# Kernel optimization log

Hardware: AMD Instinct MI355X
Metric: run time of the kernel (lower is better)

## Reference

```python
import jax, jax.numpy as jnp
import numpy as np
from jax import lax


def _sobel3d_kernels():
    # Standard separable 3D Sobel: derivative d=[-1,0,1] along one axis,
    # smoothing s=[1,2,1] along the other two. Axes order (D, H, W).
    d = np.array([-1.0, 0.0, 1.0], dtype=np.float32)
    s = np.array([1.0, 2.0, 1.0], dtype=np.float32)
    kx = np.einsum('i,j,k->ijk', d, s, s)  # derivative along D
    ky = np.einsum('i,j,k->ijk', s, d, s)  # derivative along H
    kz = np.einsum('i,j,k->ijk', s, s, d)  # derivative along W
    # Stack as [Cout=3, Cin=1, 3, 3, 3] -> one conv computes x,y,z grads at once.
    return jnp.asarray(np.stack([kx, ky, kz])[:, None])


_DN = ('NCDHW', 'OIDHW', 'NCDHW')


def _conv3(x, k):
    # x: [N, 1, D, H, W], k: [3, 1, 3, 3, 3] -> [N, 3, D-2, H-2, W-2]
    # torch F.conv3d and lax conv are both cross-correlation; VALID padding.
    return lax.conv_general_dilated(x, k, (1, 1, 1), 'VALID', dimension_numbers=_DN)


def _g2(inp, k):
    # inp: [B, D, H, W, C] (channels last, as the torch module permutes)
    b, dd, hh, ww, c = inp.shape
    x = jnp.transpose(inp, (0, 4, 1, 2, 3)).reshape(b * c, 1, dd, hh, ww)
    g1 = _conv3(x, k)                                  # [B*C, 3, D-2, H-2, W-2]
    mag = jnp.sqrt(jnp.sum(g1 * g1, axis=1, keepdims=True))  # first-order magnitude
    g2 = _conv3(mag, k)                                # [B*C, 3, D-4, H-4, W-4]
    gx, gy, gz = g2[:, 0], g2[:, 1], g2[:, 2]
    # Faithful to source: sqrt(x^2 + y^2) + z^2 (note: z is squared, not inside sqrt)
    out = jnp.sqrt(gx * gx + gy * gy) + gz * gz        # [B*C, D-4, H-4, W-4]
    return out.reshape(b, c, *out.shape[1:])


def setup_inputs() -> dict:
    key = jax.random.key(0)
    k1, k2 = jax.random.split(key)
    pred = jax.random.normal(k1, (2, 64, 64, 64, 32), dtype=jnp.float32)
    hr = jax.random.normal(k2, (2, 64, 64, 64, 32), dtype=jnp.float32)
    return {'pred': pred, 'hr': hr}


def reference(pred, hr):
    k = _sobel3d_kernels()
    return jnp.mean(jnp.abs(_g2(pred, k) - _g2(hr, k)))
```

## Files before the change

kernel.cpp:

```cpp
#include <hip/hip_runtime.h>
#include <hip/hip_fp16.h>


constexpr int BDIM = 256;
constexpr size_t IN_B = 8388608;
constexpr int IN_D = 131072;
constexpr int IN_H = 2048;
constexpr int M = 62;
constexpr int F = 60;
constexpr int C = 32;
constexpr int MROW = M * C;
constexpr size_t MAGSZ = (size_t)M * M * MROW;
constexpr size_t PLANE = (size_t)M * MROW;

__device__ __forceinline__ float2 ld2(const float* p) {
    return *reinterpret_cast<const float2*>(p);
}
__device__ __forceinline__ float2 ldh2(const __half* p) {
    return __half22float2(*reinterpret_cast<const __half2*>(p));
}

struct P1W { float2 A[4], B[4], C[4]; };

__device__ __forceinline__ void p1_plane(const float* __restrict__ col, size_t zoff,
                                         const int jr[6], P1W& W)
{
    float2 SX[6], DX[6];
#pragma unroll
    for (int j = 0; j < 6; ++j) {
        const float* p = col + zoff + jr[j];
        float2 a = ld2(p), b = ld2(p + C), c = ld2(p + 2 * C);
        SX[j] = make_float2(a.x + 2.f * b.x + c.x, a.y + 2.f * b.y + c.y);
        DX[j] = make_float2(c.x - a.x, c.y - a.y);
    }
#pragma unroll
    for (int k = 0; k < 4; ++k) {
        W.A[k] = make_float2(SX[k].x + 2.f * SX[k+1].x + SX[k+2].x,
                             SX[k].y + 2.f * SX[k+1].y + SX[k+2].y);
        W.B[k] = make_float2(SX[k+2].x - SX[k].x, SX[k+2].y - SX[k].y);
        W.C[k] = make_float2(DX[k].x + 2.f * DX[k+1].x + DX[k+2].x,
                             DX[k].y + 2.f * DX[k+1].y + DX[k+2].y);
    }
}

__device__ __forceinline__ void p1_emit(const P1W& W0, const P1W& W1, const P1W& W2,
                                        __half* __restrict__ mag, size_t cb,
                                        int z, int y0, int kmax, bool xok)
{
    if (!xok) return;
#pragma unroll
    for (int k = 0; k < 4; ++k) {
        if (k < kmax) {
            float gxx = W2.A[k].x - W0.A[k].x;
            float gxy = W2.A[k].y - W0.A[k].y;
            float gyx = W0.B[k].x + 2.f * W1.B[k].x + W2.B[k].x;
            float gyy = W0.B[k].y + 2.f * W1.B[k].y + W2.B[k].y;
            float gzx = W0.C[k].x + 2.f * W1.C[k].x + W2.C[k].x;
            float gzy = W0.C[k].y + 2.f * W1.C[k].y + W2.C[k].y;
            float mx = sqrtf(gxx * gxx + gyx * gyx + gzx * gzx);
            float my = sqrtf(gxy * gxy + gyy * gyy + gzy * gzy);
            *reinterpret_cast<__half2*>(mag + ((size_t)z * M + (y0 + k)) * MROW + cb)
                = __floats2half2_rn(mx, my);
        }
    }
}

__global__ __launch_bounds__(BDIM) void sobel_mag_stream(
    const float* __restrict__ pred, const float* __restrict__ hr,
    __half* __restrict__ magbase, int bstart)
{
    const int xt = blockIdx.x & 3, yt = blockIdx.x >> 2;
    const int zc = blockIdx.y;
    const int gz = blockIdx.z;
    const int b  = bstart + (gz >> 1);
    const float* __restrict__ in  = (gz & 1) ? hr : pred;
    __half*      __restrict__ mag = magbase + (size_t)gz * MAGSZ;

    const int y0 = yt * 4;
    const int z0 = zc * 4;
    const int zn = min(4, M - z0);
    const int kmax = min(4, M - y0);
    const int xraw = xt * 16 + (threadIdx.x >> 4);
    const bool xok = xraw < M;
    const int x = min(xraw, M - 1);
    const int c2 = (threadIdx.x & 15) << 1;

    int jr[6];
#pragma unroll
    for (int j = 0; j < 6; ++j) jr[j] = min(y0 + j, 63) * IN_H;

    const float* col = in + (size_t)b * IN_B + (size_t)x * C + c2;
    const size_t cb = (size_t)x * C + c2;

    P1W W0, W1, W2;
    p1_plane(col, (size_t)(z0 + 0) * IN_D, jr, W0);
    p1_plane(col, (size_t)(z0 + 1) * IN_D, jr, W1);
    int z = 0;
    while (true) {
        p1_plane(col, (size_t)(z0 + z + 2) * IN_D, jr, W2);
        p1_emit(W0, W1, W2, mag, cb, z0 + z, y0, kmax, xok);
        if (++z >= zn) break;
        p1_plane(col, (size_t)(z0 + z + 2) * IN_D, jr, W0);
        p1_emit(W1, W2, W0, mag, cb, z0 + z, y0, kmax, xok);
        if (++z >= zn) break;
        p1_plane(col, (size_t)(z0 + z + 2) * IN_D, jr, W1);
        p1_emit(W2, W0, W1, mag, cb, z0 + z, y0, kmax, xok);
        if (++z >= zn) break;
    }
}

struct P2W { float2 A[2], B[2], C[2]; };

__device__ __forceinline__ void p2_plane(const __half* __restrict__ col, size_t zoff, P2W& W)
{
    float2 SX[4], DX[4];
#pragma unroll
    for (int j = 0; j < 4; ++j) {
        const __half* p = col + zoff + (size_t)j * MROW;
        float2 a = ldh2(p), b = ldh2(p + C), c = ldh2(p + 2 * C);
        SX[j] = make_float2(a.x + 2.f * b.x + c.x, a.y + 2.f * b.y + c.y);
        DX[j] = make_float2(c.x - a.x, c.y - a.y);
    }
#pragma unroll
    for (int k = 0; k < 2; ++k) {
        W.A[k] = make_float2(SX[k].x + 2.f * SX[k+1].x + SX[k+2].x,
                             SX[k].y + 2.f * SX[k+1].y + SX[k+2].y);
        W.B[k] = make_float2(SX[k+2].x - SX[k].x, SX[k+2].y - SX[k].y);
        W.C[k] = make_float2(DX[k].x + 2.f * DX[k+1].x + DX[k+2].x,
                             DX[k].y + 2.f * DX[k+1].y + DX[k+2].y);
    }
}

__device__ __forceinline__ void p2_emit(const P2W& P0, const P2W& P1, const P2W& P2,
                                        const P2W& H0, const P2W& H1, const P2W& H2,
                                        float& acc)
{
#pragma unroll
    for (int k = 0; k < 2; ++k) {
        float gxPx = P2.A[k].x - P0.A[k].x;
        float gxPy = P2.A[k].y - P0.A[k].y;
        float gyPx = P0.B[k].x + 2.f * P1.B[k].x + P2.B[k].x;
        float gyPy = P0.B[k].y + 2.f * P1.B[k].y + P2.B[k].y;
        float gzPx = P0.C[k].x + 2.f * P1.C[k].x + P2.C[k].x;
        float gzPy = P0.C[k].y + 2.f * P1.C[k].y + P2.C[k].y;
        float gxHx = H2.A[k].x - H0.A[k].x;
        float gxHy = H2.A[k].y - H0.A[k].y;
        float gyHx = H0.B[k].x + 2.f * H1.B[k].x + H2.B[k].x;
        float gyHy = H0.B[k].y + 2.f * H1.B[k].y + H2.B[k].y;
        float gzHx = H0.C[k].x + 2.f * H1.C[k].x + H2.C[k].x;
        float gzHy = H0.C[k].y + 2.f * H1.C[k].y + H2.C[k].y;
        float oPx = sqrtf(gxPx * gxPx + gyPx * gyPx) + gzPx * gzPx;
        float oPy = sqrtf(gxPy * gxPy + gyPy * gyPy) + gzPy * gzPy;
        float oHx = sqrtf(gxHx * gxHx + gyHx * gyHx) + gzHx * gzHx;
        float oHy = sqrtf(gxHy * gxHy + gyHy * gyHy) + gzHy * gzHy;
        acc += fabsf(oPx - oHx) + fabsf(oPy - oHy);
    }
}

__global__ __launch_bounds__(BDIM) void sobel2_stream(
    const __half* __restrict__ magbase, float* __restrict__ partial, int bstart)
{
    const int xt = blockIdx.x & 3, yt = blockIdx.x >> 2;
    const int zc = blockIdx.y;
    const int b  = bstart + blockIdx.z;
    const __half* __restrict__ magP = magbase + (size_t)(2 * blockIdx.z) * MAGSZ;
    const __half* __restrict__ magH = magP + MAGSZ;
    const int y0 = yt * 2;
    const int z0 = zc * 4;
    const int xraw = xt * 16 + (threadIdx.x >> 4);
    const bool xok = xraw < F;
    const int x = min(xraw, F - 1);
    const int c2 = (threadIdx.x & 15) << 1;

    const size_t colo = (size_t)y0 * MROW + (size_t)x * C + c2;
    const __half* colP = magP + colo;
    const __half* colH = magH + colo;

    P2W P0, P1, P2, H0, H1, H2;
    p2_plane(colP, (size_t)(z0 + 0) * PLANE, P0);
    p2_plane(colH, (size_t)(z0 + 0) * PLANE, H0);
    p2_plane(colP, (size_t)(z0 + 1) * PLANE, P1);
    p2_plane(colH, (size_t)(z0 + 1) * PLANE, H1);
    float acc = 0.f;
    int z = 0;
    while (true) {
        p2_plane(colP, (size_t)(z0 + z + 2) * PLANE, P2);
        p2_plane(colH, (size_t)(z0 + z + 2) * PLANE, H2);
        if (xok) p2_emit(P0, P1, P2, H0, H1, H2, acc);
        if (++z >= 4) break;
        p2_plane(colP, (size_t)(z0 + z + 2) * PLANE, P0);
        p2_plane(colH, (size_t)(z0 + z + 2) * PLANE, H0);
        if (xok) p2_emit(P1, P2, P0, H1, H2, H0, acc);
        if (++z >= 4) break;
        p2_plane(colP, (size_t)(z0 + z + 2) * PLANE, P1);
        p2_plane(colH, (size_t)(z0 + z + 2) * PLANE, H1);
        if (xok) p2_emit(P2, P0, P1, H2, H0, H1, acc);
        if (++z >= 4) break;
    }

    for (int o = 32; o > 0; o >>= 1) acc += __shfl_down(acc, o, 64);
    __shared__ float sred[BDIM / 64];
    const int lane = threadIdx.x & 63, wv = threadIdx.x >> 6;
    if (lane == 0) sred[wv] = acc;
    __syncthreads();
    if (threadIdx.x == 0) {
        float t = 0.f;
#pragma unroll
        for (int i = 0; i < BDIM / 64; ++i) t += sred[i];
        partial[(size_t)b * 1800 + (size_t)zc * 120 + blockIdx.x] = t;
    }
}

__global__ __launch_bounds__(BDIM) void finalize_kernel(
    const float* __restrict__ partial, float* __restrict__ out)
{
    double a = 0.0;
    for (int i = threadIdx.x; i < 3600; i += BDIM) a += (double)partial[i];
    for (int o = 32; o > 0; o >>= 1) a += __shfl_down(a, o, 64);
    __shared__ double sd[BDIM / 64];
    const int lane = threadIdx.x & 63, wv = threadIdx.x >> 6;
    if (lane == 0) sd[wv] = a;
    __syncthreads();
    if (threadIdx.x == 0) {
        double t = 0.0;
#pragma unroll
        for (int i = 0; i < BDIM / 64; ++i) t += sd[i];
        out[0] = (float)(t / 13824000.0);
    }
}

extern "C" void kernel_launch(void* const* d_in, const int* in_sizes, int n_in,
                              void* d_out, int out_size, void* d_ws, size_t ws_size,
                              hipStream_t stream)
{
    const float* pred = (const float*)d_in[0];
    const float* hr   = (const float*)d_in[1];

    float* partial = (float*)d_ws;
    __half* magbase = (__half*)((char*)d_ws + 65536);

    const bool merged = ws_size >= (size_t)65536 + 4 * MAGSZ * sizeof(__half);
    if (merged) {
        sobel_mag_stream<<<dim3(64, 16, 4), BDIM, 0, stream>>>(pred, hr, magbase, 0);
        sobel2_stream<<<dim3(120, 15, 2), BDIM, 0, stream>>>(magbase, partial, 0);
    } else {
        for (int b = 0; b < 2; ++b) {
            sobel_mag_stream<<<dim3(64, 16, 2), BDIM, 0, stream>>>(pred, hr, magbase, b);
            sobel2_stream<<<dim3(120, 15, 1), BDIM, 0, stream>>>(magbase, partial, b);
        }
    }
    finalize_kernel<<<1, BDIM, 0, stream>>>(partial, (float*)d_out);
}
```

Before: 247.6 us.

## Software-prefetch next z-plane loads and retile both Sobel stream kernels

Both stencil kernels now split each plane's work into an issue step (raw global loads into registers) and a reduce step. The next plane's loads are issued before the current output is computed, so memory latency overlaps with arithmetic. Tiling also changes: pass 1 goes from 4 y-rows by 4 z-planes to 2 y-rows by 8 z-planes (grid 124x8), and pass 2 from 4 to 6 z-planes (grid 120x10), with partial indexing adjusted to match. Fewer y-rows per block means more redundant halo reads in y, and the extra prefetch registers may lower occupancy.

```diff
diff --git a/kernel.cpp b/kernel.cpp
--- a/kernel.cpp
+++ b/kernel.cpp
@@ -16,52 +16,58 @@
 __device__ __forceinline__ float2 ld2(const float* p) {
     return *reinterpret_cast<const float2*>(p);
 }
-__device__ __forceinline__ float2 ldh2(const __half* p) {
-    return __half22float2(*reinterpret_cast<const __half2*>(p));
-}
-
-struct P1W { float2 A[4], B[4], C[4]; };
-
-__device__ __forceinline__ void p1_plane(const float* __restrict__ col, size_t zoff,
-                                         const int jr[6], P1W& W)
-{
-    float2 SX[6], DX[6];
-#pragma unroll
-    for (int j = 0; j < 6; ++j) {
-        const float* p = col + zoff + jr[j];
-        float2 a = ld2(p), b = ld2(p + C), c = ld2(p + 2 * C);
+
+struct Raw1 { float2 v[12]; };
+struct P1W  { float2 A[2], B[2], Cc[2]; };
+
+__device__ __forceinline__ void p1_issue(const float* __restrict__ pbase,
+                                         int zplane, int y0, int lo, Raw1& r)
+{
+#pragma unroll
+    for (int j = 0; j < 4; ++j) {
+        const float* rowp = pbase + (size_t)zplane * IN_D + (size_t)(y0 + j) * IN_H;
+        r.v[j * 3 + 0] = ld2(rowp + lo);
+        r.v[j * 3 + 1] = ld2(rowp + lo + C);
+        r.v[j * 3 + 2] = ld2(rowp + lo + 2 * C);
+    }
+}
+
+__device__ __forceinline__ void p1_reduce(const Raw1& r, P1W& W)
+{
+    float2 SX[4], DX[4];
+#pragma unroll
+    for (int j = 0; j < 4; ++j) {
+        float2 a = r.v[j * 3], b = r.v[j * 3 + 1], c = r.v[j * 3 + 2];
         SX[j] = make_float2(a.x + 2.f * b.x + c.x, a.y + 2.f * b.y + c.y);
         DX[j] = make_float2(c.x - a.x, c.y - a.y);
     }
 #pragma unroll
-    for (int k = 0; k < 4; ++k) {
-        W.A[k] = make_float2(SX[k].x + 2.f * SX[k+1].x + SX[k+2].x,
-                             SX[k].y + 2.f * SX[k+1].y + SX[k+2].y);
-        W.B[k] = make_float2(SX[k+2].x - SX[k].x, SX[k+2].y - SX[k].y);
-        W.C[k] = make_float2(DX[k].x + 2.f * DX[k+1].x + DX[k+2].x,
-                             DX[k].y + 2.f * DX[k+1].y + DX[k+2].y);
+    for (int k = 0; k < 2; ++k) {
+        W.A[k]  = make_float2(SX[k].x + 2.f * SX[k+1].x + SX[k+2].x,
+                              SX[k].y + 2.f * SX[k+1].y + SX[k+2].y);
+        W.B[k]  = make_float2(SX[k+2].x - SX[k].x, SX[k+2].y - SX[k].y);
+        W.Cc[k] = make_float2(DX[k].x + 2.f * DX[k+1].x + DX[k+2].x,
+                              DX[k].y + 2.f * DX[k+1].y + DX[k+2].y);
     }
 }
 
 __device__ __forceinline__ void p1_emit(const P1W& W0, const P1W& W1, const P1W& W2,
-                                        __half* __restrict__ mag, size_t cb,
-                                        int z, int y0, int kmax, bool xok)
+                                        __half* __restrict__ mag, int z, int y0,
+                                        int lo, bool xok)
 {
     if (!xok) return;
 #pragma unroll
-    for (int k = 0; k < 4; ++k) {
-        if (k < kmax) {
-            float gxx = W2.A[k].x - W0.A[k].x;
-            float gxy = W2.A[k].y - W0.A[k].y;
-            float gyx = W0.B[k].x + 2.f * W1.B[k].x + W2.B[k].x;
-            float gyy = W0.B[k].y + 2.f * W1.B[k].y + W2.B[k].y;
-            float gzx = W0.C[k].x + 2.f * W1.C[k].x + W2.C[k].x;
-            float gzy = W0.C[k].y + 2.f * W1.C[k].y + W2.C[k].y;
-            float mx = sqrtf(gxx * gxx + gyx * gyx + gzx * gzx);
-            float my = sqrtf(gxy * gxy + gyy * gyy + gzy * gzy);
-            *reinterpret_cast<__half2*>(mag + ((size_t)z * M + (y0 + k)) * MROW + cb)
-                = __floats2half2_rn(mx, my);
-        }
+    for (int k = 0; k < 2; ++k) {
+        float gxx = W2.A[k].x - W0.A[k].x;
+        float gxy = W2.A[k].y - W0.A[k].y;
+        float gyx = W0.B[k].x + 2.f * W1.B[k].x + W2.B[k].x;
+        float gyy = W0.B[k].y + 2.f * W1.B[k].y + W2.B[k].y;
+        float gzx = W0.Cc[k].x + 2.f * W1.Cc[k].x + W2.Cc[k].x;
+        float gzy = W0.Cc[k].y + 2.f * W1.Cc[k].y + W2.Cc[k].y;
+        float mx = sqrtf(gxx * gxx + gyx * gyx + gzx * gzx);
+        float my = sqrtf(gxy * gxy + gyy * gyy + gzy * gzy);
+        *reinterpret_cast<__half2*>(mag + ((size_t)z * M + (y0 + k)) * MROW + lo)
+            = __floats2half2_rn(mx, my);
     }
 }
 
@@ -76,58 +82,77 @@
     const float* __restrict__ in  = (gz & 1) ? hr : pred;
     __half*      __restrict__ mag = magbase + (size_t)gz * MAGSZ;
 
-    const int y0 = yt * 4;
-    const int z0 = zc * 4;
-    const int zn = min(4, M - z0);
-    const int kmax = min(4, M - y0);
+    const int y0 = yt * 2;
+    const int z0 = zc * 8;
+    const int zn = min(8, M - z0);
     const int xraw = xt * 16 + (threadIdx.x >> 4);
     const bool xok = xraw < M;
     const int x = min(xraw, M - 1);
-    const int c2 = (threadIdx.x & 15) << 1;
-
-    int jr[6];
-#pragma unroll
-    for (int j = 0; j < 6; ++j) jr[j] = min(y0 + j, 63) * IN_H;
-
-    const float* col = in + (size_t)b * IN_B + (size_t)x * C + c2;
-    const size_t cb = (size_t)x * C + c2;
-
+    const int lo = x * C + ((threadIdx.x & 15) << 1);
+
+    const float* pbase = in + (size_t)b * IN_B;
+
+    Raw1 r;
     P1W W0, W1, W2;
-    p1_plane(col, (size_t)(z0 + 0) * IN_D, jr, W0);
-    p1_plane(col, (size_t)(z0 + 1) * IN_D, jr, W1);
+    p1_issue(pbase, z0 + 0, y0, lo, r); p1_reduce(r, W0);
+    p1_issue(pbase, z0 + 1, y0, lo, r); p1_reduce(r, W1);
+    p1_issue(pbase, z0 + 2, y0, lo, r); p1_reduce(r, W2);
     int z = 0;
-    while (true) {
-        p1_plane(col, (size_t)(z0 + z + 2) * IN_D, jr, W2);
-        p1_emit(W0, W1, W2, mag, cb, z0 + z, y0, kmax, xok);
-        if (++z >= zn) break;
-        p1_plane(col, (size_t)(z0 + z + 2) * IN_D, jr, W0);
-        p1_emit(W1, W2, W0, mag, cb, z0 + z, y0, kmax, xok);
-        if (++z >= zn) break;
-        p1_plane(col, (size_t)(z0 + z + 2) * IN_D, jr, W1);
-        p1_emit(W2, W0, W1, mag, cb, z0 + z, y0, kmax, xok);
-        if (++z >= zn) break;
-    }
-}
-
-struct P2W { float2 A[2], B[2], C[2]; };
-
-__device__ __forceinline__ void p2_plane(const __half* __restrict__ col, size_t zoff, P2W& W)
+    for (;;) {
+        bool more = (z + 1 < zn);
+        if (more) p1_issue(pbase, z0 + z + 3, y0, lo, r);
+        p1_emit(W0, W1, W2, mag, z0 + z, y0, lo, xok);
+        if (!more) break;
+        ++z;
+        p1_reduce(r, W0);
+        more = (z + 1 < zn);
+        if (more) p1_issue(pbase, z0 + z + 3, y0, lo, r);
+        p1_emit(W1, W2, W0, mag, z0 + z, y0, lo, xok);
+        if (!more) break;
+        ++z;
+        p1_reduce(r, W1);
+        more = (z + 1 < zn);
+        if (more) p1_issue(pbase, z0 + z + 3, y0, lo, r);
+        p1_emit(W2, W0, W1, mag, z0 + z, y0, lo, xok);
+        if (!more) break;
+        ++z;
+        p1_reduce(r, W2);
+    }
+}
+
+struct Raw2 { __half2 v[12]; };
+struct P2W  { float2 A[2], B[2], Cc[2]; };
+
+__device__ __forceinline__ void p2_issue(const __half* __restrict__ mbase,
+                                         int zplane, int y0, int lo, Raw2& r)
+{
+#pragma unroll
+    for (int j = 0; j < 4; ++j) {
+        const __half* rowp = mbase + (size_t)zplane * PLANE + (size_t)(y0 + j) * MROW;
+        r.v[j * 3 + 0] = *reinterpret_cast<const __half2*>(rowp + lo);
+        r.v[j * 3 + 1] = *reinterpret_cast<const __half2*>(rowp + lo + C);
+        r.v[j * 3 + 2] = *reinterpret_cast<const __half2*>(rowp + lo + 2 * C);
+    }
+}
+
+__device__ __forceinline__ void p2_reduce(const Raw2& r, P2W& W)
 {
     float2 SX[4], DX[4];
 #pragma unroll
     for (int j = 0; j < 4; ++j) {
-        const __half* p = col + zoff + (size_t)j * MROW;
-        float2 a = ldh2(p), b = ldh2(p + C), c = ldh2(p + 2 * C);
+        float2 a = __half22float2(r.v[j * 3]);
+        float2 b = __half22float2(r.v[j * 3 + 1]);
+        float2 c = __half22float2(r.v[j * 3 + 2]);
         SX[j] = make_float2(a.x + 2.f * b.x + c.x, a.y + 2.f * b.y + c.y);
         DX[j] = make_float2(c.x - a.x, c.y - a.y);
     }
 #pragma unroll
     for (int k = 0; k < 2; ++k) {
-        W.A[k] = make_float2(SX[k].x + 2.f * SX[k+1].x + SX[k+2].x,
-                             SX[k].y + 2.f * SX[k+1].y + SX[k+2].y);
-        W.B[k] = make_float2(SX[k+2].x - SX[k].x, SX[k+2].y - SX[k].y);
-        W.C[k] = make_float2(DX[k].x + 2.f * DX[k+1].x + DX[k+2].x,
-                             DX[k].y + 2.f * DX[k+1].y + DX[k+2].y);
+        W.A[k]  = make_float2(SX[k].x + 2.f * SX[k+1].x + SX[k+2].x,
+                              SX[k].y + 2.f * SX[k+1].y + SX[k+2].y);
+        W.B[k]  = make_float2(SX[k+2].x - SX[k].x, SX[k+2].y - SX[k].y);
+        W.Cc[k] = make_float2(DX[k].x + 2.f * DX[k+1].x + DX[k+2].x,
+                              DX[k].y + 2.f * DX[k+1].y + DX[k+2].y);
     }
 }
 
@@ -141,14 +166,14 @@
         float gxPy = P2.A[k].y - P0.A[k].y;
         float gyPx = P0.B[k].x + 2.f * P1.B[k].x + P2.B[k].x;
         float gyPy = P0.B[k].y + 2.f * P1.B[k].y + P2.B[k].y;
-        float gzPx = P0.C[k].x + 2.f * P1.C[k].x + P2.C[k].x;
-        float gzPy = P0.C[k].y + 2.f * P1.C[k].y + P2.C[k].y;
+        float gzPx = P0.Cc[k].x + 2.f * P1.Cc[k].x + P2.Cc[k].x;
+        float gzPy = P0.Cc[k].y + 2.f * P1.Cc[k].y + P2.Cc[k].y;
         float gxHx = H2.A[k].x - H0.A[k].x;
         float gxHy = H2.A[k].y - H0.A[k].y;
         float gyHx = H0.B[k].x + 2.f * H1.B[k].x + H2.B[k].x;
         float gyHy = H0.B[k].y + 2.f * H1.B[k].y + H2.B[k].y;
-        float gzHx = H0.C[k].x + 2.f * H1.C[k].x + H2.C[k].x;
-        float gzHy = H0.C[k].y + 2.f * H1.C[k].y + H2.C[k].y;
+        float gzHx = H0.Cc[k].x + 2.f * H1.Cc[k].x + H2.Cc[k].x;
+        float gzHy = H0.Cc[k].y + 2.f * H1.Cc[k].y + H2.Cc[k].y;
         float oPx = sqrtf(gxPx * gxPx + gyPx * gyPx) + gzPx * gzPx;
         float oPy = sqrtf(gxPy * gxPy + gyPy * gyPy) + gzPy * gzPy;
         float oHx = sqrtf(gxHx * gxHx + gyHx * gyHx) + gzHx * gzHx;
@@ -165,37 +190,48 @@
     const int b  = bstart + blockIdx.z;
     const __half* __restrict__ magP = magbase + (size_t)(2 * blockIdx.z) * MAGSZ;
     const __half* __restrict__ magH = magP + MAGSZ;
+
     const int y0 = yt * 2;
-    const int z0 = zc * 4;
+    const int z0 = zc * 6;
+    const int zn = 6;
     const int xraw = xt * 16 + (threadIdx.x >> 4);
     const bool xok = xraw < F;
     const int x = min(xraw, F - 1);
-    const int c2 = (threadIdx.x & 15) << 1;
-
-    const size_t colo = (size_t)y0 * MROW + (size_t)x * C + c2;
-    const __half* colP = magP + colo;
-    const __half* colH = magH + colo;
-
+    const int lo = x * C + ((threadIdx.x & 15) << 1);
+
+    Raw2 rp, rh;
     P2W P0, P1, P2, H0, H1, H2;
-    p2_plane(colP, (size_t)(z0 + 0) * PLANE, P0);
-    p2_plane(colH, (size_t)(z0 + 0) * PLANE, H0);
-    p2_plane(colP, (size_t)(z0 + 1) * PLANE, P1);
-    p2_plane(colH, (size_t)(z0 + 1) * PLANE, H1);
+    p2_issue(magP, z0 + 0, y0, lo, rp); p2_issue(magH, z0 + 0, y0, lo, rh);
+    p2_reduce(rp, P0); p2_reduce(rh, H0);
+    p2_issue(magP, z0 + 1, y0, lo, rp); p2_issue(magH, z0 + 1, y0, lo, rh);
+    p2_reduce(rp, P1); p2_reduce(rh, H1);
+    p2_issue(magP, z0 + 2, y0, lo, rp); p2_issue(magH, z0 + 2, y0, lo, rh);
+    p2_reduce(rp, P2); p2_reduce(rh, H2);
+
     float acc = 0.f;
     int z = 0;
-    while (true) {
-        p2_plane(colP, (size_t)(z0 + z + 2) * PLANE, P2);
-        p2_plane(colH, (size_t)(z0 + z + 2) * PLANE, H2);
+    for (;;) {
+        bool more = (z + 1 < zn);
+        if (more) { p2_issue(magP, z0 + z + 3, y0, lo, rp);
+                    p2_issue(magH, z0 + z + 3, y0, lo, rh); }
         if (xok) p2_emit(P0, P1, P2, H0, H1, H2, acc);
-        if (++z >= 4) break;
-        p2_plane(colP, (size_t)(z0 + z + 2) * PLANE, P0);
-        p2_plane(colH, (size_t)(z0 + z + 2) * PLANE, H0);
+        if (!more) break;
+        ++z;
+        p2_reduce(rp, P0); p2_reduce(rh, H0);
+        more = (z + 1 < zn);
+        if (more) { p2_issue(magP, z0 + z + 3, y0, lo, rp);
+                    p2_issue(magH, z0 + z + 3, y0, lo, rh); }
         if (xok) p2_emit(P1, P2, P0, H1, H2, H0, acc);
-        if (++z >= 4) break;
-        p2_plane(colP, (size_t)(z0 + z + 2) * PLANE, P1);
-        p2_plane(colH, (size_t)(z0 + z + 2) * PLANE, H1);
+        if (!more) break;
+        ++z;
+        p2_reduce(rp, P1); p2_reduce(rh, H1);
+        more = (z + 1 < zn);
+        if (more) { p2_issue(magP, z0 + z + 3, y0, lo, rp);
+                    p2_issue(magH, z0 + z + 3, y0, lo, rh); }
         if (xok) p2_emit(P2, P0, P1, H2, H0, H1, acc);
-        if (++z >= 4) break;
+        if (!more) break;
+        ++z;
+        p2_reduce(rp, P2); p2_reduce(rh, H2);
     }
 
     for (int o = 32; o > 0; o >>= 1) acc += __shfl_down(acc, o, 64);
@@ -207,7 +243,7 @@
         float t = 0.f;
 #pragma unroll
         for (int i = 0; i < BDIM / 64; ++i) t += sred[i];
-        partial[(size_t)b * 1800 + (size_t)zc * 120 + blockIdx.x] = t;
+        partial[(size_t)b * 1200 + (size_t)zc * 120 + blockIdx.x] = t;
     }
 }
 
@@ -215,7 +251,7 @@
     const float* __restrict__ partial, float* __restrict__ out)
 {
     double a = 0.0;
-    for (int i = threadIdx.x; i < 3600; i += BDIM) a += (double)partial[i];
+    for (int i = threadIdx.x; i < 2400; i += BDIM) a += (double)partial[i];
     for (int o = 32; o > 0; o >>= 1) a += __shfl_down(a, o, 64);
     __shared__ double sd[BDIM / 64];
     const int lane = threadIdx.x & 63, wv = threadIdx.x >> 6;
@@ -241,12 +277,12 @@
 
     const bool merged = ws_size >= (size_t)65536 + 4 * MAGSZ * sizeof(__half);
     if (merged) {
-        sobel_mag_stream<<<dim3(64, 16, 4), BDIM, 0, stream>>>(pred, hr, magbase, 0);
-        sobel2_stream<<<dim3(120, 15, 2), BDIM, 0, stream>>>(magbase, partial, 0);
+        sobel_mag_stream<<<dim3(124, 8, 4), BDIM, 0, stream>>>(pred, hr, magbase, 0);
+        sobel2_stream<<<dim3(120, 10, 2), BDIM, 0, stream>>>(magbase, partial, 0);
     } else {
         for (int b = 0; b < 2; ++b) {
-            sobel_mag_stream<<<dim3(64, 16, 2), BDIM, 0, stream>>>(pred, hr, magbase, b);
-            sobel2_stream<<<dim3(120, 15, 1), BDIM, 0, stream>>>(magbase, partial, b);
+            sobel_mag_stream<<<dim3(124, 8, 2), BDIM, 0, stream>>>(pred, hr, magbase, b);
+            sobel2_stream<<<dim3(120, 10, 1), BDIM, 0, stream>>>(magbase, partial, b);
         }
     }
     finalize_kernel<<<1, BDIM, 0, stream>>>(partial, (float*)d_out);
```

Result: slower. 253.1 us (+2.2%).

## Stage input planes through LDS and lengthen z-chunks in both Sobel passes

Applied to the files above, without the earlier changes.

Both stencil kernels now cooperatively load each z-plane tile (with x/y halo) into padded shared memory using wide vector loads, then each thread reads its 3x3 neighbourhood from LDS instead of issuing redundant overlapping global loads. Z-chunk length grows from 4 to 8 in the first pass and 6 in the second, reducing halo re-reads across blocks, and the partial-sum grid shrinks to match. This cuts global-memory traffic and redundant loads, but adds two block barriers per plane and serialises load and compute with no double buffering. It also reduces the number of blocks, which lowers occupancy and parallelism.

```diff
diff --git a/kernel.cpp b/kernel.cpp
--- a/kernel.cpp
+++ b/kernel.cpp
@@ -13,62 +13,91 @@
 constexpr size_t MAGSZ = (size_t)M * M * MROW;
 constexpr size_t PLANE = (size_t)M * MROW;
 
-__device__ __forceinline__ float2 ld2(const float* p) {
-    return *reinterpret_cast<const float2*>(p);
-}
-__device__ __forceinline__ float2 ldh2(const __half* p) {
-    return __half22float2(*reinterpret_cast<const __half2*>(p));
-}
-
-struct P1W { float2 A[4], B[4], C[4]; };
-
-__device__ __forceinline__ void p1_plane(const float* __restrict__ col, size_t zoff,
-                                         const int jr[6], P1W& W)
+constexpr int GS1 = 34;
+constexpr int RS1 = 18 * GS1;
+constexpr int GS2 = 36;
+constexpr int RS2 = 18 * GS2;
+constexpr int VS2 = 4 * RS2;
+
+__device__ __forceinline__ float2 sm3(float2 a, float2 b, float2 c) {
+    return make_float2(a.x + 2.f * b.x + c.x, a.y + 2.f * b.y + c.y);
+}
+__device__ __forceinline__ float2 df2(float2 a, float2 c) {
+    return make_float2(c.x - a.x, c.y - a.y);
+}
+
+struct P1W { float2 A[4], B[4], Cc[4]; };
+
+__device__ __forceinline__ void p1_stage(const float* __restrict__ pbase, int zp,
+                                         int y0, int x0, float* __restrict__ lds,
+                                         int tid)
+{
+#pragma unroll
+    for (int k = 0; k < 4; ++k) {
+        int i = tid + k * BDIM;
+        if (i < 864) {
+            int row = i / 144;
+            int rem = i - row * 144;
+            int g   = rem >> 3;
+            int off = (rem & 7) << 2;
+            int ry  = min(y0 + row, 63);
+            int gx  = min(x0 + g, 63);
+            float4 v = *reinterpret_cast<const float4*>(
+                pbase + (size_t)zp * IN_D + (size_t)ry * IN_H + gx * C + off);
+            float* d = lds + row * RS1 + g * GS1 + off;
+            *reinterpret_cast<float2*>(d)     = make_float2(v.x, v.y);
+            *reinterpret_cast<float2*>(d + 2) = make_float2(v.z, v.w);
+        }
+    }
+}
+
+__device__ __forceinline__ void p1_reduce(const float* __restrict__ lds,
+                                          int xl, int cl, P1W& W)
 {
     float2 SX[6], DX[6];
 #pragma unroll
     for (int j = 0; j < 6; ++j) {
-        const float* p = col + zoff + jr[j];
-        float2 a = ld2(p), b = ld2(p + C), c = ld2(p + 2 * C);
-        SX[j] = make_float2(a.x + 2.f * b.x + c.x, a.y + 2.f * b.y + c.y);
-        DX[j] = make_float2(c.x - a.x, c.y - a.y);
+        const float* r = lds + j * RS1 + xl * GS1 + 2 * cl;
+        float2 a = *reinterpret_cast<const float2*>(r);
+        float2 b = *reinterpret_cast<const float2*>(r + GS1);
+        float2 c = *reinterpret_cast<const float2*>(r + 2 * GS1);
+        SX[j] = sm3(a, b, c);
+        DX[j] = df2(a, c);
     }
 #pragma unroll
     for (int k = 0; k < 4; ++k) {
-        W.A[k] = make_float2(SX[k].x + 2.f * SX[k+1].x + SX[k+2].x,
-                             SX[k].y + 2.f * SX[k+1].y + SX[k+2].y);
-        W.B[k] = make_float2(SX[k+2].x - SX[k].x, SX[k+2].y - SX[k].y);
-        W.C[k] = make_float2(DX[k].x + 2.f * DX[k+1].x + DX[k+2].x,
-                             DX[k].y + 2.f * DX[k+1].y + DX[k+2].y);
+        W.A[k]  = sm3(SX[k], SX[k + 1], SX[k + 2]);
+        W.B[k]  = df2(SX[k], SX[k + 2]);
+        W.Cc[k] = sm3(DX[k], DX[k + 1], DX[k + 2]);
     }
 }
 
 __device__ __forceinline__ void p1_emit(const P1W& W0, const P1W& W1, const P1W& W2,
-                                        __half* __restrict__ mag, size_t cb,
-                                        int z, int y0, int kmax, bool xok)
-{
-    if (!xok) return;
+                                        __half* __restrict__ mag, int z, int y0,
+                                        int xo, int cl, int kmax, bool xok)
+{
 #pragma unroll
     for (int k = 0; k < 4; ++k) {
         if (k < kmax) {
-            float gxx = W2.A[k].x - W0.A[k].x;
-            float gxy = W2.A[k].y - W0.A[k].y;
-            float gyx = W0.B[k].x + 2.f * W1.B[k].x + W2.B[k].x;
-            float gyy = W0.B[k].y + 2.f * W1.B[k].y + W2.B[k].y;
-            float gzx = W0.C[k].x + 2.f * W1.C[k].x + W2.C[k].x;
-            float gzy = W0.C[k].y + 2.f * W1.C[k].y + W2.C[k].y;
-            float mx = sqrtf(gxx * gxx + gyx * gyx + gzx * gzx);
-            float my = sqrtf(gxy * gxy + gyy * gyy + gzy * gzy);
-            *reinterpret_cast<__half2*>(mag + ((size_t)z * M + (y0 + k)) * MROW + cb)
-                = __floats2half2_rn(mx, my);
+            float2 gx = df2(W0.A[k], W2.A[k]);
+            float2 gy = sm3(W0.B[k], W1.B[k], W2.B[k]);
+            float2 gz = sm3(W0.Cc[k], W1.Cc[k], W2.Cc[k]);
+            float mx = sqrtf(gx.x * gx.x + gy.x * gy.x + gz.x * gz.x);
+            float my = sqrtf(gx.y * gx.y + gy.y * gy.y + gz.y * gz.y);
+            if (xok)
+                *reinterpret_cast<__half2*>(
+                    mag + ((size_t)z * M + (y0 + k)) * MROW + xo * C + 2 * cl)
+                    = __floats2half2_rn(mx, my);
         }
     }
 }
 
-__global__ __launch_bounds__(BDIM) void sobel_mag_stream(
+__global__ __launch_bounds__(BDIM) void sobel_mag_lds(
     const float* __restrict__ pred, const float* __restrict__ hr,
     __half* __restrict__ magbase, int bstart)
 {
+    __shared__ float lds[6 * RS1];
+
     const int xt = blockIdx.x & 3, yt = blockIdx.x >> 2;
     const int zc = blockIdx.y;
     const int gz = blockIdx.z;
@@ -76,58 +105,99 @@
     const float* __restrict__ in  = (gz & 1) ? hr : pred;
     __half*      __restrict__ mag = magbase + (size_t)gz * MAGSZ;
 
-    const int y0 = yt * 4;
-    const int z0 = zc * 4;
-    const int zn = min(4, M - z0);
+    const int x0 = xt * 16, y0 = yt * 4;
+    const int z0 = zc * 8;
+    const int zn = min(8, M - z0);
     const int kmax = min(4, M - y0);
-    const int xraw = xt * 16 + (threadIdx.x >> 4);
-    const bool xok = xraw < M;
-    const int x = min(xraw, M - 1);
-    const int c2 = (threadIdx.x & 15) << 1;
-
-    int jr[6];
-#pragma unroll
-    for (int j = 0; j < 6; ++j) jr[j] = min(y0 + j, 63) * IN_H;
-
-    const float* col = in + (size_t)b * IN_B + (size_t)x * C + c2;
-    const size_t cb = (size_t)x * C + c2;
+    const int tid = threadIdx.x;
+    const int xl = tid >> 4;
+    const int cl = tid & 15;
+    const int xo = x0 + xl;
+    const bool xok = xo < M;
+
+    const float* pbase = in + (size_t)b * IN_B;
 
     P1W W0, W1, W2;
-    p1_plane(col, (size_t)(z0 + 0) * IN_D, jr, W0);
-    p1_plane(col, (size_t)(z0 + 1) * IN_D, jr, W1);
-    int z = 0;
-    while (true) {
-        p1_plane(col, (size_t)(z0 + z + 2) * IN_D, jr, W2);
-        p1_emit(W0, W1, W2, mag, cb, z0 + z, y0, kmax, xok);
-        if (++z >= zn) break;
-        p1_plane(col, (size_t)(z0 + z + 2) * IN_D, jr, W0);
-        p1_emit(W1, W2, W0, mag, cb, z0 + z, y0, kmax, xok);
-        if (++z >= zn) break;
-        p1_plane(col, (size_t)(z0 + z + 2) * IN_D, jr, W1);
-        p1_emit(W2, W0, W1, mag, cb, z0 + z, y0, kmax, xok);
-        if (++z >= zn) break;
-    }
-}
-
-struct P2W { float2 A[2], B[2], C[2]; };
-
-__device__ __forceinline__ void p2_plane(const __half* __restrict__ col, size_t zoff, P2W& W)
+    p1_stage(pbase, z0 + 0, y0, x0, lds, tid);
+    __syncthreads();
+    p1_reduce(lds, xl, cl, W0);
+    __syncthreads();
+    p1_stage(pbase, z0 + 1, y0, x0, lds, tid);
+    __syncthreads();
+    p1_reduce(lds, xl, cl, W1);
+    __syncthreads();
+
+    int zi = 2;
+    for (;;) {
+        p1_stage(pbase, z0 + zi, y0, x0, lds, tid);
+        __syncthreads();
+        p1_reduce(lds, xl, cl, W2);
+        __syncthreads();
+        p1_emit(W0, W1, W2, mag, z0 + zi - 2, y0, xo, cl, kmax, xok);
+        if (++zi >= zn + 2) break;
+
+        p1_stage(pbase, z0 + zi, y0, x0, lds, tid);
+        __syncthreads();
+        p1_reduce(lds, xl, cl, W0);
+        __syncthreads();
+        p1_emit(W1, W2, W0, mag, z0 + zi - 2, y0, xo, cl, kmax, xok);
+        if (++zi >= zn + 2) break;
+
+        p1_stage(pbase, z0 + zi, y0, x0, lds, tid);
+        __syncthreads();
+        p1_reduce(lds, xl, cl, W1);
+        __syncthreads();
+        p1_emit(W2, W0, W1, mag, z0 + zi - 2, y0, xo, cl, kmax, xok);
+        if (++zi >= zn + 2) break;
+    }
+}
+
+struct P2W { float2 A[2], B[2], Cc[2]; };
+
+__device__ __forceinline__ void p2_stage(const __half* __restrict__ magP,
+                                         const __half* __restrict__ magH,
+                                         int zp, int y0, int x0,
+                                         __half* __restrict__ lds, int tid)
+{
+#pragma unroll
+    for (int k = 0; k < 5; ++k) {
+        int i = tid + k * BDIM;
+        if (i < 1152) {
+            int vol = (i >= 576) ? 1 : 0;
+            int rem = i - vol * 576;
+            int row = rem / 144;
+            int rem2 = rem - row * 144;
+            int g   = rem2 >> 3;
+            int off = (rem2 & 7) << 2;
+            const __half* src = (vol ? magH : magP)
+                + (size_t)zp * PLANE + (size_t)(y0 + row) * MROW
+                + min(x0 + g, M - 1) * C + off;
+            uint2 v = *reinterpret_cast<const uint2*>(src);
+            unsigned* d = reinterpret_cast<unsigned*>(
+                lds + vol * VS2 + row * RS2 + g * GS2 + off);
+            d[0] = v.x; d[1] = v.y;
+        }
+    }
+}
+
+__device__ __forceinline__ void p2_reduce(const __half* __restrict__ lds,
+                                          int xl, int cl, P2W& W)
 {
     float2 SX[4], DX[4];
 #pragma unroll
     for (int j = 0; j < 4; ++j) {
-        const __half* p = col + zoff + (size_t)j * MROW;
-        float2 a = ldh2(p), b = ldh2(p + C), c = ldh2(p + 2 * C);
-        SX[j] = make_float2(a.x + 2.f * b.x + c.x, a.y + 2.f * b.y + c.y);
-        DX[j] = make_float2(c.x - a.x, c.y - a.y);
+        const __half* r = lds + j * RS2 + xl * GS2 + 2 * cl;
+        float2 a = __half22float2(*reinterpret_cast<const __half2*>(r));
+        float2 b = __half22float2(*reinterpret_cast<const __half2*>(r + GS2));
+        float2 c = __half22float2(*reinterpret_cast<const __half2*>(r + 2 * GS2));
+        SX[j] = sm3(a, b, c);
+        DX[j] = df2(a, c);
     }
 #pragma unroll
     for (int k = 0; k < 2; ++k) {
-        W.A[k] = make_float2(SX[k].x + 2.f * SX[k+1].x + SX[k+2].x,
-                             SX[k].y + 2.f * SX[k+1].y + SX[k+2].y);
-        W.B[k] = make_float2(SX[k+2].x - SX[k].x, SX[k+2].y - SX[k].y);
-        W.C[k] = make_float2(DX[k].x + 2.f * DX[k+1].x + DX[k+2].x,
-                             DX[k].y + 2.f * DX[k+1].y + DX[k+2].y);
+        W.A[k]  = sm3(SX[k], SX[k + 1], SX[k + 2]);
+        W.B[k]  = df2(SX[k], SX[k + 2]);
+        W.Cc[k] = sm3(DX[k], DX[k + 1], DX[k + 2]);
     }
 }
 
@@ -137,77 +207,83 @@
 {
 #pragma unroll
     for (int k = 0; k < 2; ++k) {
-        float gxPx = P2.A[k].x - P0.A[k].x;
-        float gxPy = P2.A[k].y - P0.A[k].y;
-        float gyPx = P0.B[k].x + 2.f * P1.B[k].x + P2.B[k].x;
-        float gyPy = P0.B[k].y + 2.f * P1.B[k].y + P2.B[k].y;
-        float gzPx = P0.C[k].x + 2.f * P1.C[k].x + P2.C[k].x;
-        float gzPy = P0.C[k].y + 2.f * P1.C[k].y + P2.C[k].y;
-        float gxHx = H2.A[k].x - H0.A[k].x;
-        float gxHy = H2.A[k].y - H0.A[k].y;
-        float gyHx = H0.B[k].x + 2.f * H1.B[k].x + H2.B[k].x;
-        float gyHy = H0.B[k].y + 2.f * H1.B[k].y + H2.B[k].y;
-        float gzHx = H0.C[k].x + 2.f * H1.C[k].x + H2.C[k].x;
-        float gzHy = H0.C[k].y + 2.f * H1.C[k].y + H2.C[k].y;
-        float oPx = sqrtf(gxPx * gxPx + gyPx * gyPx) + gzPx * gzPx;
-        float oPy = sqrtf(gxPy * gxPy + gyPy * gyPy) + gzPy * gzPy;
-        float oHx = sqrtf(gxHx * gxHx + gyHx * gyHx) + gzHx * gzHx;
-        float oHy = sqrtf(gxHy * gxHy + gyHy * gyHy) + gzHy * gzHy;
+        float2 gxP = df2(P0.A[k], P2.A[k]);
+        float2 gyP = sm3(P0.B[k], P1.B[k], P2.B[k]);
+        float2 gzP = sm3(P0.Cc[k], P1.Cc[k], P2.Cc[k]);
+        float2 gxH = df2(H0.A[k], H2.A[k]);
+        float2 gyH = sm3(H0.B[k], H1.B[k], H2.B[k]);
+        float2 gzH = sm3(H0.Cc[k], H1.Cc[k], H2.Cc[k]);
+        float oPx = sqrtf(gxP.x * gxP.x + gyP.x * gyP.x) + gzP.x * gzP.x;
+        float oPy = sqrtf(gxP.y * gxP.y + gyP.y * gyP.y) + gzP.y * gzP.y;
+        float oHx = sqrtf(gxH.x * gxH.x + gyH.x * gyH.x) + gzH.x * gzH.x;
+        float oHy = sqrtf(gxH.y * gxH.y + gyH.y * gyH.y) + gzH.y * gzH.y;
         acc += fabsf(oPx - oHx) + fabsf(oPy - oHy);
     }
 }
 
-__global__ __launch_bounds__(BDIM) void sobel2_stream(
+__global__ __launch_bounds__(BDIM) void sobel2_lds(
     const __half* __restrict__ magbase, float* __restrict__ partial, int bstart)
 {
+    __shared__ __half lds[2 * VS2];
+
     const int xt = blockIdx.x & 3, yt = blockIdx.x >> 2;
     const int zc = blockIdx.y;
     const int b  = bstart + blockIdx.z;
     const __half* __restrict__ magP = magbase + (size_t)(2 * blockIdx.z) * MAGSZ;
     const __half* __restrict__ magH = magP + MAGSZ;
-    const int y0 = yt * 2;
-    const int z0 = zc * 4;
-    const int xraw = xt * 16 + (threadIdx.x >> 4);
-    const bool xok = xraw < F;
-    const int x = min(xraw, F - 1);
-    const int c2 = (threadIdx.x & 15) << 1;
-
-    const size_t colo = (size_t)y0 * MROW + (size_t)x * C + c2;
-    const __half* colP = magP + colo;
-    const __half* colH = magH + colo;
+
+    const int x0 = xt * 16, y0 = yt * 2;
+    const int z0 = zc * 6;
+    const int tid = threadIdx.x;
+    const int xl = tid >> 4;
+    const int cl = tid & 15;
+    const bool xok = (x0 + xl) < F;
 
     P2W P0, P1, P2, H0, H1, H2;
-    p2_plane(colP, (size_t)(z0 + 0) * PLANE, P0);
-    p2_plane(colH, (size_t)(z0 + 0) * PLANE, H0);
-    p2_plane(colP, (size_t)(z0 + 1) * PLANE, P1);
-    p2_plane(colH, (size_t)(z0 + 1) * PLANE, H1);
+    p2_stage(magP, magH, z0 + 0, y0, x0, lds, tid);
+    __syncthreads();
+    p2_reduce(lds, xl, cl, P0); p2_reduce(lds + VS2, xl, cl, H0);
+    __syncthreads();
+    p2_stage(magP, magH, z0 + 1, y0, x0, lds, tid);
+    __syncthreads();
+    p2_reduce(lds, xl, cl, P1); p2_reduce(lds + VS2, xl, cl, H1);
+    __syncthreads();
+
     float acc = 0.f;
-    int z = 0;
-    while (true) {
-        p2_plane(colP, (size_t)(z0 + z + 2) * PLANE, P2);
-        p2_plane(colH, (size_t)(z0 + z + 2) * PLANE, H2);
+    int zi = 2;
+    for (;;) {
+        p2_stage(magP, magH, z0 + zi, y0, x0, lds, tid);
+        __syncthreads();
+        p2_reduce(lds, xl, cl, P2); p2_reduce(lds + VS2, xl, cl, H2);
+        __syncthreads();
         if (xok) p2_emit(P0, P1, P2, H0, H1, H2, acc);
-        if (++z >= 4) break;
-        p2_plane(colP, (size_t)(z0 + z + 2) * PLANE, P0);
-        p2_plane(colH, (size_t)(z0 + z + 2) * PLANE, H0);
+        if (++zi >= 8) break;
+
+        p2_stage(magP, magH, z0 + zi, y0, x0, lds, tid);
+        __syncthreads();
+        p2_reduce(lds, xl, cl, P0); p2_reduce(lds + VS2, xl, cl, H0);
+        __syncthreads();
         if (xok) p2_emit(P1, P2, P0, H1, H2, H0, acc);
-        if (++z >= 4) break;
-        p2_plane(colP, (size_t)(z0 + z + 2) * PLANE, P1);
-        p2_plane(colH, (size_t)(z0 + z + 2) * PLANE, H1);
+        if (++zi >= 8) break;
+
+        p2_stage(magP, magH, z0 + zi, y0, x0, lds, tid);
+        __syncthreads();
+        p2_reduce(lds, xl, cl, P1); p2_reduce(lds + VS2, xl, cl, H1);
+        __syncthreads();
         if (xok) p2_emit(P2, P0, P1, H2, H0, H1, acc);
-        if (++z >= 4) break;
+        if (++zi >= 8) break;
     }
 
     for (int o = 32; o > 0; o >>= 1) acc += __shfl_down(acc, o, 64);
     __shared__ float sred[BDIM / 64];
-    const int lane = threadIdx.x & 63, wv = threadIdx.x >> 6;
+    const int lane = tid & 63, wv = tid >> 6;
     if (lane == 0) sred[wv] = acc;
     __syncthreads();
-    if (threadIdx.x == 0) {
+    if (tid == 0) {
         float t = 0.f;
 #pragma unroll
         for (int i = 0; i < BDIM / 64; ++i) t += sred[i];
-        partial[(size_t)b * 1800 + (size_t)zc * 120 + blockIdx.x] = t;
+        partial[(size_t)b * 1200 + (size_t)zc * 120 + blockIdx.x] = t;
     }
 }
 
@@ -215,7 +291,7 @@
     const float* __restrict__ partial, float* __restrict__ out)
 {
     double a = 0.0;
-    for (int i = threadIdx.x; i < 3600; i += BDIM) a += (double)partial[i];
+    for (int i = threadIdx.x; i < 2400; i += BDIM) a += (double)partial[i];
     for (int o = 32; o > 0; o >>= 1) a += __shfl_down(a, o, 64);
     __shared__ double sd[BDIM / 64];
     const int lane = threadIdx.x & 63, wv = threadIdx.x >> 6;
@@ -241,12 +317,12 @@
 
     const bool merged = ws_size >= (size_t)65536 + 4 * MAGSZ * sizeof(__half);
     if (merged) {
-        sobel_mag_stream<<<dim3(64, 16, 4), BDIM, 0, stream>>>(pred, hr, magbase, 0);
-        sobel2_stream<<<dim3(120, 15, 2), BDIM, 0, stream>>>(magbase, partial, 0);
+        sobel_mag_lds<<<dim3(64, 8, 4), BDIM, 0, stream>>>(pred, hr, magbase, 0);
+        sobel2_lds<<<dim3(120, 10, 2), BDIM, 0, stream>>>(magbase, partial, 0);
     } else {
         for (int b = 0; b < 2; ++b) {
-            sobel_mag_stream<<<dim3(64, 16, 2), BDIM, 0, stream>>>(pred, hr, magbase, b);
-            sobel2_stream<<<dim3(120, 15, 1), BDIM, 0, stream>>>(magbase, partial, b);
+            sobel_mag_lds<<<dim3(64, 8, 2), BDIM, 0, stream>>>(pred, hr, magbase, b);
+            sobel2_lds<<<dim3(120, 10, 1), BDIM, 0, stream>>>(magbase, partial, b);
         }
     }
     finalize_kernel<<<1, BDIM, 0, stream>>>(partial, (float*)d_out);
```

After: 288.4 us. 1.16x slower.
